# Kernel tuning notes

Hardware: AMD Instinct MI355X
Metric: run time of the kernel (lower is better)

The kernel has to match this reference:

```python
import jax, jax.numpy as jnp
import numpy as np

N_ATOMS = 768
BOX_L = 30.0
CUTOFF = 5.0


def _cp(a, b, c):
    # numpy equivalent of torch.cartesian_prod for 1-D inputs
    g = np.meshgrid(a, b, c, indexing='ij')
    return np.stack(g, axis=-1).reshape(-1, 3)


def get_shifts_np(box, pbc, cutoff):
    # host-side mirror of TorchNeighborList._get_shifts (data-dependent shapes)
    recip = np.linalg.inv(box).T
    inv_len = np.linalg.norm(recip, axis=1)
    nrep = np.where(pbc, np.ceil(cutoff * inv_len).astype(np.int64), 0)
    r1 = np.arange(1, nrep[0] + 1)
    r2 = np.arange(1, nrep[1] + 1)
    r3 = np.arange(1, nrep[2] + 1)
    o = np.zeros(1, dtype=np.int64)
    blocks = [_cp(r1, r2, r3), _cp(r1, r2, o), _cp(r1, r2, -r3),
              _cp(r1, o, r3), _cp(r1, o, o), _cp(r1, o, -r3),
              _cp(r1, -r2, r3), _cp(r1, -r2, o), _cp(r1, -r2, -r3),
              _cp(o, r2, r3), _cp(o, r2, o), _cp(o, r2, -r3), _cp(o, o, r3)]
    return np.concatenate(blocks, axis=0).astype(np.int32)


def setup_inputs() -> dict:
    key = jax.random.key(0)
    positions = jax.random.uniform(key, (N_ATOMS, 3), dtype=jnp.float32) * BOX_L
    box = jnp.eye(3, dtype=jnp.float32) * BOX_L
    shifts = jnp.asarray(get_shifts_np(np.eye(3) * BOX_L, np.array([True, True, True]), CUTOFF))  # (13, 3)
    return {"positions": positions, "box": box, "shifts": shifts, "cutoff": CUTOFF}


def reference(positions, box, shifts, cutoff):
    N = positions.shape[0]
    S = shifts.shape[0]
    # central-cell unique pairs i<j (torch.combinations)
    iu, ju = jnp.triu_indices(N, k=1)
    # shifted candidates: cartesian_prod(shift_index, i, j)
    shift_idx = jnp.repeat(jnp.arange(S), N * N)
    pi_s = jnp.tile(jnp.repeat(jnp.arange(N), N), S)
    pj_s = jnp.tile(jnp.arange(N), S * N)
    pi_all = jnp.concatenate([iu, pi_s])          # (P,)
    pj_all = jnp.concatenate([ju, pj_s])          # (P,)
    shifts_all = jnp.concatenate([jnp.zeros((iu.shape[0], 3), dtype=shifts.dtype), shifts[shift_idx]])  # (P,3)
    shift_vals = shifts_all.astype(box.dtype) @ box
    Rij = positions[pi_all] - positions[pj_all] + shift_vals  # (P,3)
    d = jnp.linalg.norm(Rij, axis=1)
    mask = d < cutoff
    # bidirectional pairs (torch.cat of (i,j) and (j,i)), offsets negated for the first half
    bi_i = jnp.concatenate([pi_all, pj_all])
    bi_j = jnp.concatenate([pj_all, pi_all])
    bi_off = jnp.concatenate([-shifts_all, shifts_all])
    bi_mask = jnp.concatenate([mask, mask])
    # jit-compatible compaction: sort by idx_i with invalid entries pushed to the end
    sort_key = jnp.where(bi_mask, bi_i, N)
    order = jnp.argsort(sort_key)  # jax sort is stable
    valid = bi_mask[order]
    idx_i = jnp.where(valid, bi_i[order], -1)
    idx_j = jnp.where(valid, bi_j[order], -1)
    offset = (bi_off[order].astype(box.dtype) @ box) * valid[:, None].astype(box.dtype)
    return idx_i, idx_j, offset, valid
```

## Files before the change

kernel.cpp:

```cpp
#include <hip/hip_runtime.h>

#pragma clang fp contract(off)


#define MAX_SHIFTS 64
#define NFB 4096

typedef float f32x4 __attribute__((ext_vector_type(4)));
typedef int i32x4 __attribute__((ext_vector_type(4)));

__device__ __forceinline__ bool pv_fwd(float fx, float fy, float fz,
                                       const float* __restrict__ pos, int j,
                                       float sx, float sy, float sz, float cutoff) {
  float dx = fx - pos[j * 3 + 0] + sx;
  float dy = fy - pos[j * 3 + 1] + sy;
  float dz = fz - pos[j * 3 + 2] + sz;
  float d2 = dx * dx + dy * dy + dz * dz;
  return sqrtf(d2) < cutoff;
}

__device__ __forceinline__ bool pv_bwd(const float* __restrict__ pos, int a,
                                       float fx, float fy, float fz,
                                       float sx, float sy, float sz, float cutoff) {
  float dx = pos[a * 3 + 0] - fx + sx;
  float dy = pos[a * 3 + 1] - fy + sy;
  float dz = pos[a * 3 + 2] - fz + sz;
  float d2 = dx * dx + dy * dy + dz * dz;
  return sqrtf(d2) < cutoff;
}

__device__ __forceinline__ bool axis_ok(float lo, float hi, float cutpad) {
  return (hi > -cutpad) && (lo < cutpad);
}

__global__ __launch_bounds__(256) void k_count(
    const float* __restrict__ pos, const float* __restrict__ box,
    const int* __restrict__ shifts, const float* __restrict__ cutp,
    int N, int S, int* __restrict__ count) {
  __shared__ float sv[MAX_SHIFTS * 3];
  __shared__ float bred[4][6];
  __shared__ int rf[4], rb[4];
  int atom = blockIdx.x;
  int t = threadIdx.x;
  int w = t >> 6;
  float cut = cutp[0];
  float cutpad = cut + fmaxf(cut * 1e-5f, 1e-5f);

  for (int s = t; s < S; s += 256) {
    float s0 = (float)shifts[s * 3 + 0];
    float s1 = (float)shifts[s * 3 + 1];
    float s2 = (float)shifts[s * 3 + 2];
    sv[s * 3 + 0] = s0 * box[0] + s1 * box[3] + s2 * box[6];
    sv[s * 3 + 1] = s0 * box[1] + s1 * box[4] + s2 * box[7];
    sv[s * 3 + 2] = s0 * box[2] + s1 * box[5] + s2 * box[8];
  }

  float mnx = 1e30f, mny = 1e30f, mnz = 1e30f, mxx = -1e30f, mxy = -1e30f, mxz = -1e30f;
  for (int i = t; i < N; i += 256) {
    float x = pos[3 * i + 0], y = pos[3 * i + 1], z = pos[3 * i + 2];
    mnx = fminf(mnx, x); mny = fminf(mny, y); mnz = fminf(mnz, z);
    mxx = fmaxf(mxx, x); mxy = fmaxf(mxy, y); mxz = fmaxf(mxz, z);
  }
  for (int off = 32; off; off >>= 1) {
    mnx = fminf(mnx, __shfl_xor(mnx, off)); mny = fminf(mny, __shfl_xor(mny, off));
    mnz = fminf(mnz, __shfl_xor(mnz, off)); mxx = fmaxf(mxx, __shfl_xor(mxx, off));
    mxy = fmaxf(mxy, __shfl_xor(mxy, off)); mxz = fmaxf(mxz, __shfl_xor(mxz, off));
  }
  if ((t & 63) == 0) {
    bred[w][0] = mnx; bred[w][1] = mny; bred[w][2] = mnz;
    bred[w][3] = mxx; bred[w][4] = mxy; bred[w][5] = mxz;
  }
  __syncthreads();
  mnx = bred[0][0]; mny = bred[0][1]; mnz = bred[0][2];
  mxx = bred[0][3]; mxy = bred[0][4]; mxz = bred[0][5];
  for (int ww = 1; ww < 4; ww++) {
    mnx = fminf(mnx, bred[ww][0]); mny = fminf(mny, bred[ww][1]); mnz = fminf(mnz, bred[ww][2]);
    mxx = fmaxf(mxx, bred[ww][3]); mxy = fmaxf(mxy, bred[ww][4]); mxz = fmaxf(mxz, bred[ww][5]);
  }

  float pix = pos[3 * atom + 0], piy = pos[3 * atom + 1], piz = pos[3 * atom + 2];
  int cf = 0, cb = 0;
  for (int j = atom + 1 + t; j < N; j += 256)
    if (pv_fwd(pix, piy, piz, pos, j, 0.f, 0.f, 0.f, cut)) cf++;
  for (int a = t; a < atom; a += 256)
    if (pv_bwd(pos, a, pix, piy, piz, 0.f, 0.f, 0.f, cut)) cb++;

  for (int s = 0; s < S; s++) {
    float svx = sv[3 * s + 0], svy = sv[3 * s + 1], svz = sv[3 * s + 2];
    bool af = axis_ok((pix - mxx) + svx, (pix - mnx) + svx, cutpad) &&
              axis_ok((piy - mxy) + svy, (piy - mny) + svy, cutpad) &&
              axis_ok((piz - mxz) + svz, (piz - mnz) + svz, cutpad);
    if (af) {
      for (int j = t; j < N; j += 256)
        if (pv_fwd(pix, piy, piz, pos, j, svx, svy, svz, cut)) cf++;
    }
    bool ab = axis_ok((mnx - pix) + svx, (mxx - pix) + svx, cutpad) &&
              axis_ok((mny - piy) + svy, (mxy - piy) + svy, cutpad) &&
              axis_ok((mnz - piz) + svz, (mxz - piz) + svz, cutpad);
    if (ab) {
      for (int a = t; a < N; a += 256)
        if (pv_bwd(pos, a, pix, piy, piz, svx, svy, svz, cut)) cb++;
    }
  }
  for (int off = 32; off; off >>= 1) {
    cf += __shfl_down(cf, off);
    cb += __shfl_down(cb, off);
  }
  if ((t & 63) == 0) { rf[w] = cf; rb[w] = cb; }
  __syncthreads();
  if (t == 0) {
    count[2 * atom + 0] = rf[0] + rf[1] + rf[2] + rf[3];
    count[2 * atom + 1] = rb[0] + rb[1] + rb[2] + rb[3];
  }
}

__global__ __launch_bounds__(256) void k_main(
    const float* __restrict__ pos, const float* __restrict__ box,
    const int* __restrict__ shifts, const float* __restrict__ cutp,
    int N, int S, const int* __restrict__ count,
    float* __restrict__ out, long M, long n4, int NWB) {
  __shared__ float sv[MAX_SHIFTS * 3];
  int t = threadIdx.x;
  int lane = t & 63, w = t >> 6;
  int n2 = 2 * N;

  if ((int)blockIdx.x < NWB) {
    float cut = cutp[0];
    float cutpad = cut + fmaxf(cut * 1e-5f, 1e-5f);
    for (int s = t; s < S; s += 256) {
      float s0 = (float)shifts[s * 3 + 0];
      float s1 = (float)shifts[s * 3 + 1];
      float s2 = (float)shifts[s * 3 + 2];
      sv[s * 3 + 0] = s0 * box[0] + s1 * box[3] + s2 * box[6];
      sv[s * 3 + 1] = s0 * box[1] + s1 * box[4] + s2 * box[7];
      sv[s * 3 + 2] = s0 * box[2] + s1 * box[5] + s2 * box[8];
    }
    __syncthreads();
    int g = blockIdx.x * 4 + w;
    if (g >= n2) return;
    int atom = g >> 1;
    int dir = g & 1;

    float mnx = 1e30f, mny = 1e30f, mnz = 1e30f, mxx = -1e30f, mxy = -1e30f, mxz = -1e30f;
    for (int i = lane; i < N; i += 64) {
      float x = pos[3 * i + 0], y = pos[3 * i + 1], z = pos[3 * i + 2];
      mnx = fminf(mnx, x); mny = fminf(mny, y); mnz = fminf(mnz, z);
      mxx = fmaxf(mxx, x); mxy = fmaxf(mxy, y); mxz = fmaxf(mxz, z);
    }
    for (int off = 32; off; off >>= 1) {
      mnx = fminf(mnx, __shfl_xor(mnx, off)); mny = fminf(mny, __shfl_xor(mny, off));
      mnz = fminf(mnz, __shfl_xor(mnz, off)); mxx = fmaxf(mxx, __shfl_xor(mxx, off));
      mxy = fmaxf(mxy, __shfl_xor(mxy, off)); mxz = fmaxf(mxz, __shfl_xor(mxz, off));
    }

    int pre = 0;
    for (int i = lane; i < g; i += 64) pre += count[i];
    for (int off = 32; off; off >>= 1) pre += __shfl_xor(pre, off);
    long base = pre;

    float* __restrict__ out_i = out;
    float* __restrict__ out_j = out + M;
    float* __restrict__ out_off = out + 2 * M;
    float* __restrict__ out_v = out + 5 * M;

    float pix = pos[3 * atom + 0], piy = pos[3 * atom + 1], piz = pos[3 * atom + 2];
    float fatom = (float)atom;
    float cut2 = cut;
    int running = 0;

    {
      int n = (dir == 0) ? (N - 1 - atom) : atom;
      int j0 = (dir == 0) ? (atom + 1) : 0;
      float oz0 = (dir == 0) ? -0.0f : 0.0f;
      for (int c0 = 0; c0 < n; c0 += 64) {
        int c = c0 + lane;
        bool v = false;
        int other = j0 + c;
        if (c < n) {
          v = (dir == 0) ? pv_fwd(pix, piy, piz, pos, other, 0.f, 0.f, 0.f, cut2)
                         : pv_bwd(pos, other, pix, piy, piz, 0.f, 0.f, 0.f, cut2);
        }
        unsigned long long m = __ballot(v);
        if (v) {
          int rank = __popcll(m & ((1ULL << lane) - 1ULL));
          long row = base + running + rank;
          out_i[row] = fatom;
          out_j[row] = (float)other;
          out_off[row * 3 + 0] = oz0;
          out_off[row * 3 + 1] = oz0;
          out_off[row * 3 + 2] = oz0;
          out_v[row] = 1.0f;
        }
        running += __popcll(m);
      }
    }
    for (int s = 0; s < S; s++) {
      float svx = sv[3 * s + 0], svy = sv[3 * s + 1], svz = sv[3 * s + 2];
      bool active;
      if (dir == 0) {
        active = axis_ok((pix - mxx) + svx, (pix - mnx) + svx, cutpad) &&
                 axis_ok((piy - mxy) + svy, (piy - mny) + svy, cutpad) &&
                 axis_ok((piz - mxz) + svz, (piz - mnz) + svz, cutpad);
      } else {
        active = axis_ok((mnx - pix) + svx, (mxx - pix) + svx, cutpad) &&
                 axis_ok((mny - piy) + svy, (mxy - piy) + svy, cutpad) &&
                 axis_ok((mnz - piz) + svz, (mxz - piz) + svz, cutpad);
      }
      if (!active) continue;
      float ox = (dir == 0) ? -svx : svx;
      float oy = (dir == 0) ? -svy : svy;
      float oz = (dir == 0) ? -svz : svz;
      for (int c0 = 0; c0 < N; c0 += 64) {
        int other = c0 + lane;
        bool v = false;
        if (other < N) {
          v = (dir == 0) ? pv_fwd(pix, piy, piz, pos, other, svx, svy, svz, cut2)
                         : pv_bwd(pos, other, pix, piy, piz, svx, svy, svz, cut2);
        }
        unsigned long long m = __ballot(v);
        if (v) {
          int rank = __popcll(m & ((1ULL << lane) - 1ULL));
          long row = base + running + rank;
          out_i[row] = fatom;
          out_j[row] = (float)other;
          out_off[row * 3 + 0] = ox;
          out_off[row * 3 + 1] = oy;
          out_off[row * 3 + 2] = oz;
          out_v[row] = 1.0f;
        }
        running += __popcll(m);
      }
    }
  } else {
    int tot = 0;
    const i32x4* __restrict__ c4 = (const i32x4*)count;
    int nq = n2 >> 2;
    for (int i = lane; i < nq; i += 64) {
      i32x4 v = c4[i];
      tot += v.x + v.y + v.z + v.w;
    }
    for (int off = 32; off; off >>= 1) tot += __shfl_xor(tot, off);
    long total = tot;

    long E0 = total;
    long E1 = M + total;
    long E2 = 2 * M + 3 * total;
    long E3 = 5 * M + total;
    long m2 = 2 * M, m5 = 5 * M;
    const f32x4 neg = {-1.f, -1.f, -1.f, -1.f};
    const f32x4 zer = {0.f, 0.f, 0.f, 0.f};
    f32x4* __restrict__ out4 = (f32x4*)out;

    long fidx = ((long)blockIdx.x - NWB) * 256 + t;
    long fstride = (long)NFB * 256;
    for (long k = fidx; k < n4; k += fstride) {
      long e = k << 2;
      long ve = (e < M) ? E0 : ((e < m2) ? E1 : ((e < m5) ? E2 : E3));
      if (e + 4 <= ve) continue;
      bool isneg = (e < m2);
      if (e >= ve) {
        out4[k] = isneg ? neg : zer;
      } else {
        float dv = isneg ? -1.f : 0.f;
        for (int q = 0; q < 4; q++)
          if (e + q >= ve) out[e + q] = dv;
      }
    }
  }
}

extern "C" void kernel_launch(void* const* d_in, const int* in_sizes, int n_in,
                              void* d_out, int out_size, void* d_ws, size_t ws_size,
                              hipStream_t stream) {
  const float* pos = (const float*)d_in[0];
  const float* box = (const float*)d_in[1];
  const int* shifts = (const int*)d_in[2];
  const float* cutp = (const float*)d_in[3];
  int N = in_sizes[0] / 3;
  int S = in_sizes[2] / 3;
  long M = (long)out_size / 6;
  float* out = (float*)d_out;

  int* count = (int*)d_ws;

  long n4 = (long)out_size / 4;
  int NWB = (2 * N + 3) / 4;

  hipLaunchKernelGGL(k_count, dim3(N), dim3(256), 0, stream,
                     pos, box, shifts, cutp, N, S, count);
  hipLaunchKernelGGL(k_main, dim3(NWB + NFB), dim3(256), 0, stream,
                     pos, box, shifts, cutp, N, S, count, out, M, n4, NWB);
}
```

Baseline: 110.3 us.

## Reorder fill blocks first and give each a contiguous chunk with fast path

The fill blocks now come first in the grid, and there are fewer of them. Each one handles a contiguous, 256-aligned chunk of the output instead of grid-striding across the whole buffer. Chunks that do not overlap any valid region or segment boundary take a branch-free unrolled vector-store loop that writes a constant value. This cuts per-element branching and index arithmetic in the large padding fill and lets the fill start earlier. The risk is load imbalance across fewer blocks, and pair blocks that are scheduled later could lengthen the tail.

```diff
diff --git a/kernel.cpp b/kernel.cpp
--- a/kernel.cpp
+++ b/kernel.cpp
@@ -4,7 +4,7 @@
 
 
 #define MAX_SHIFTS 64
-#define NFB 4096
+#define NFB 512
 
 typedef float f32x4 __attribute__((ext_vector_type(4)));
 typedef int i32x4 __attribute__((ext_vector_type(4)));
@@ -118,120 +118,18 @@
     const float* __restrict__ pos, const float* __restrict__ box,
     const int* __restrict__ shifts, const float* __restrict__ cutp,
     int N, int S, const int* __restrict__ count,
-    float* __restrict__ out, long M, long n4, int NWB) {
+    float* __restrict__ out, long M, long n4, long chunk4) {
   __shared__ float sv[MAX_SHIFTS * 3];
   int t = threadIdx.x;
   int lane = t & 63, w = t >> 6;
   int n2 = 2 * N;
 
-  if ((int)blockIdx.x < NWB) {
-    float cut = cutp[0];
-    float cutpad = cut + fmaxf(cut * 1e-5f, 1e-5f);
-    for (int s = t; s < S; s += 256) {
-      float s0 = (float)shifts[s * 3 + 0];
-      float s1 = (float)shifts[s * 3 + 1];
-      float s2 = (float)shifts[s * 3 + 2];
-      sv[s * 3 + 0] = s0 * box[0] + s1 * box[3] + s2 * box[6];
-      sv[s * 3 + 1] = s0 * box[1] + s1 * box[4] + s2 * box[7];
-      sv[s * 3 + 2] = s0 * box[2] + s1 * box[5] + s2 * box[8];
-    }
-    __syncthreads();
-    int g = blockIdx.x * 4 + w;
-    if (g >= n2) return;
-    int atom = g >> 1;
-    int dir = g & 1;
-
-    float mnx = 1e30f, mny = 1e30f, mnz = 1e30f, mxx = -1e30f, mxy = -1e30f, mxz = -1e30f;
-    for (int i = lane; i < N; i += 64) {
-      float x = pos[3 * i + 0], y = pos[3 * i + 1], z = pos[3 * i + 2];
-      mnx = fminf(mnx, x); mny = fminf(mny, y); mnz = fminf(mnz, z);
-      mxx = fmaxf(mxx, x); mxy = fmaxf(mxy, y); mxz = fmaxf(mxz, z);
-    }
-    for (int off = 32; off; off >>= 1) {
-      mnx = fminf(mnx, __shfl_xor(mnx, off)); mny = fminf(mny, __shfl_xor(mny, off));
-      mnz = fminf(mnz, __shfl_xor(mnz, off)); mxx = fmaxf(mxx, __shfl_xor(mxx, off));
-      mxy = fmaxf(mxy, __shfl_xor(mxy, off)); mxz = fmaxf(mxz, __shfl_xor(mxz, off));
-    }
-
-    int pre = 0;
-    for (int i = lane; i < g; i += 64) pre += count[i];
-    for (int off = 32; off; off >>= 1) pre += __shfl_xor(pre, off);
-    long base = pre;
-
-    float* __restrict__ out_i = out;
-    float* __restrict__ out_j = out + M;
-    float* __restrict__ out_off = out + 2 * M;
-    float* __restrict__ out_v = out + 5 * M;
-
-    float pix = pos[3 * atom + 0], piy = pos[3 * atom + 1], piz = pos[3 * atom + 2];
-    float fatom = (float)atom;
-    float cut2 = cut;
-    int running = 0;
-
-    {
-      int n = (dir == 0) ? (N - 1 - atom) : atom;
-      int j0 = (dir == 0) ? (atom + 1) : 0;
-      float oz0 = (dir == 0) ? -0.0f : 0.0f;
-      for (int c0 = 0; c0 < n; c0 += 64) {
-        int c = c0 + lane;
-        bool v = false;
-        int other = j0 + c;
-        if (c < n) {
-          v = (dir == 0) ? pv_fwd(pix, piy, piz, pos, other, 0.f, 0.f, 0.f, cut2)
-                         : pv_bwd(pos, other, pix, piy, piz, 0.f, 0.f, 0.f, cut2);
-        }
-        unsigned long long m = __ballot(v);
-        if (v) {
-          int rank = __popcll(m & ((1ULL << lane) - 1ULL));
-          long row = base + running + rank;
-          out_i[row] = fatom;
-          out_j[row] = (float)other;
-          out_off[row * 3 + 0] = oz0;
-          out_off[row * 3 + 1] = oz0;
-          out_off[row * 3 + 2] = oz0;
-          out_v[row] = 1.0f;
-        }
-        running += __popcll(m);
-      }
-    }
-    for (int s = 0; s < S; s++) {
-      float svx = sv[3 * s + 0], svy = sv[3 * s + 1], svz = sv[3 * s + 2];
-      bool active;
-      if (dir == 0) {
-        active = axis_ok((pix - mxx) + svx, (pix - mnx) + svx, cutpad) &&
-                 axis_ok((piy - mxy) + svy, (piy - mny) + svy, cutpad) &&
-                 axis_ok((piz - mxz) + svz, (piz - mnz) + svz, cutpad);
-      } else {
-        active = axis_ok((mnx - pix) + svx, (mxx - pix) + svx, cutpad) &&
-                 axis_ok((mny - piy) + svy, (mxy - piy) + svy, cutpad) &&
-                 axis_ok((mnz - piz) + svz, (mxz - piz) + svz, cutpad);
-      }
-      if (!active) continue;
-      float ox = (dir == 0) ? -svx : svx;
-      float oy = (dir == 0) ? -svy : svy;
-      float oz = (dir == 0) ? -svz : svz;
-      for (int c0 = 0; c0 < N; c0 += 64) {
-        int other = c0 + lane;
-        bool v = false;
-        if (other < N) {
-          v = (dir == 0) ? pv_fwd(pix, piy, piz, pos, other, svx, svy, svz, cut2)
-                         : pv_bwd(pos, other, pix, piy, piz, svx, svy, svz, cut2);
-        }
-        unsigned long long m = __ballot(v);
-        if (v) {
-          int rank = __popcll(m & ((1ULL << lane) - 1ULL));
-          long row = base + running + rank;
-          out_i[row] = fatom;
-          out_j[row] = (float)other;
-          out_off[row * 3 + 0] = ox;
-          out_off[row * 3 + 1] = oy;
-          out_off[row * 3 + 2] = oz;
-          out_v[row] = 1.0f;
-        }
-        running += __popcll(m);
-      }
-    }
-  } else {
+  if ((int)blockIdx.x < NFB) {
+    long k_lo = (long)blockIdx.x * chunk4;
+    long k_hi = k_lo + chunk4;
+    if (k_hi > n4) k_hi = n4;
+    if (k_lo >= k_hi) return;
+
     int tot = 0;
     const i32x4* __restrict__ c4 = (const i32x4*)count;
     int nq = n2 >> 2;
@@ -251,20 +149,141 @@
     const f32x4 zer = {0.f, 0.f, 0.f, 0.f};
     f32x4* __restrict__ out4 = (f32x4*)out;
 
-    long fidx = ((long)blockIdx.x - NWB) * 256 + t;
-    long fstride = (long)NFB * 256;
-    for (long k = fidx; k < n4; k += fstride) {
-      long e = k << 2;
-      long ve = (e < M) ? E0 : ((e < m2) ? E1 : ((e < m5) ? E2 : E3));
-      if (e + 4 <= ve) continue;
-      bool isneg = (e < m2);
-      if (e >= ve) {
-        out4[k] = isneg ? neg : zer;
-      } else {
-        float dv = isneg ? -1.f : 0.f;
-        for (int q = 0; q < 4; q++)
-          if (e + q >= ve) out[e + q] = dv;
-      }
+    long e_lo = k_lo << 2, e_hi = k_hi << 2;
+    bool crosses = (e_lo < m2) && (e_hi > m2);
+    bool ov = (e_lo < E0) ||
+              (e_hi > M && e_lo < E1) ||
+              (e_hi > m2 && e_lo < E2) ||
+              (e_hi > m5 && e_lo < E3);
+
+    if (!crosses && !ov) {
+      f32x4 val = (e_lo < m2) ? neg : zer;
+      f32x4* __restrict__ p = out4 + k_lo + t;
+      long iters = (k_hi - k_lo) >> 8;
+#pragma unroll 8
+      for (long it = 0; it < iters; it++) p[it * 256] = val;
+      for (long k = k_lo + (iters << 8) + t; k < k_hi; k += 256) out4[k] = (k << 2) < m2 ? neg : zer;
+    } else {
+      for (long k = k_lo + t; k < k_hi; k += 256) {
+        long e = k << 2;
+        long ve = (e < M) ? E0 : ((e < m2) ? E1 : ((e < m5) ? E2 : E3));
+        if (e + 4 <= ve) continue;
+        bool isneg = (e < m2);
+        if (e >= ve) {
+          out4[k] = isneg ? neg : zer;
+        } else {
+          float dv = isneg ? -1.f : 0.f;
+          for (int q = 0; q < 4; q++)
+            if (e + q >= ve) out[e + q] = dv;
+        }
+      }
+    }
+    return;
+  }
+
+  float cut = cutp[0];
+  float cutpad = cut + fmaxf(cut * 1e-5f, 1e-5f);
+  for (int s = t; s < S; s += 256) {
+    float s0 = (float)shifts[s * 3 + 0];
+    float s1 = (float)shifts[s * 3 + 1];
+    float s2 = (float)shifts[s * 3 + 2];
+    sv[s * 3 + 0] = s0 * box[0] + s1 * box[3] + s2 * box[6];
+    sv[s * 3 + 1] = s0 * box[1] + s1 * box[4] + s2 * box[7];
+    sv[s * 3 + 2] = s0 * box[2] + s1 * box[5] + s2 * box[8];
+  }
+  __syncthreads();
+  int g = ((int)blockIdx.x - NFB) * 4 + w;
+  if (g >= n2) return;
+  int atom = g >> 1;
+  int dir = g & 1;
+
+  float mnx = 1e30f, mny = 1e30f, mnz = 1e30f, mxx = -1e30f, mxy = -1e30f, mxz = -1e30f;
+  for (int i = lane; i < N; i += 64) {
+    float x = pos[3 * i + 0], y = pos[3 * i + 1], z = pos[3 * i + 2];
+    mnx = fminf(mnx, x); mny = fminf(mny, y); mnz = fminf(mnz, z);
+    mxx = fmaxf(mxx, x); mxy = fmaxf(mxy, y); mxz = fmaxf(mxz, z);
+  }
+  for (int off = 32; off; off >>= 1) {
+    mnx = fminf(mnx, __shfl_xor(mnx, off)); mny = fminf(mny, __shfl_xor(mny, off));
+    mnz = fminf(mnz, __shfl_xor(mnz, off)); mxx = fmaxf(mxx, __shfl_xor(mxx, off));
+    mxy = fmaxf(mxy, __shfl_xor(mxy, off)); mxz = fmaxf(mxz, __shfl_xor(mxz, off));
+  }
+
+  int pre = 0;
+  for (int i = lane; i < g; i += 64) pre += count[i];
+  for (int off = 32; off; off >>= 1) pre += __shfl_xor(pre, off);
+  long base = pre;
+
+  float* __restrict__ out_i = out;
+  float* __restrict__ out_j = out + M;
+  float* __restrict__ out_off = out + 2 * M;
+  float* __restrict__ out_v = out + 5 * M;
+
+  float pix = pos[3 * atom + 0], piy = pos[3 * atom + 1], piz = pos[3 * atom + 2];
+  float fatom = (float)atom;
+  int running = 0;
+
+  {
+    int n = (dir == 0) ? (N - 1 - atom) : atom;
+    int j0 = (dir == 0) ? (atom + 1) : 0;
+    float oz0 = (dir == 0) ? -0.0f : 0.0f;
+    for (int c0 = 0; c0 < n; c0 += 64) {
+      int c = c0 + lane;
+      bool v = false;
+      int other = j0 + c;
+      if (c < n) {
+        v = (dir == 0) ? pv_fwd(pix, piy, piz, pos, other, 0.f, 0.f, 0.f, cut)
+                       : pv_bwd(pos, other, pix, piy, piz, 0.f, 0.f, 0.f, cut);
+      }
+      unsigned long long m = __ballot(v);
+      if (v) {
+        int rank = __popcll(m & ((1ULL << lane) - 1ULL));
+        long row = base + running + rank;
+        out_i[row] = fatom;
+        out_j[row] = (float)other;
+        out_off[row * 3 + 0] = oz0;
+        out_off[row * 3 + 1] = oz0;
+        out_off[row * 3 + 2] = oz0;
+        out_v[row] = 1.0f;
+      }
+      running += __popcll(m);
+    }
+  }
+  for (int s = 0; s < S; s++) {
+    float svx = sv[3 * s + 0], svy = sv[3 * s + 1], svz = sv[3 * s + 2];
+    bool active;
+    if (dir == 0) {
+      active = axis_ok((pix - mxx) + svx, (pix - mnx) + svx, cutpad) &&
+               axis_ok((piy - mxy) + svy, (piy - mny) + svy, cutpad) &&
+               axis_ok((piz - mxz) + svz, (piz - mnz) + svz, cutpad);
+    } else {
+      active = axis_ok((mnx - pix) + svx, (mxx - pix) + svx, cutpad) &&
+               axis_ok((mny - piy) + svy, (mxy - piy) + svy, cutpad) &&
+               axis_ok((mnz - piz) + svz, (mxz - piz) + svz, cutpad);
+    }
+    if (!active) continue;
+    float ox = (dir == 0) ? -svx : svx;
+    float oy = (dir == 0) ? -svy : svy;
+    float oz = (dir == 0) ? -svz : svz;
+    for (int c0 = 0; c0 < N; c0 += 64) {
+      int other = c0 + lane;
+      bool v = false;
+      if (other < N) {
+        v = (dir == 0) ? pv_fwd(pix, piy, piz, pos, other, svx, svy, svz, cut)
+                       : pv_bwd(pos, other, pix, piy, piz, svx, svy, svz, cut);
+      }
+      unsigned long long m = __ballot(v);
+      if (v) {
+        int rank = __popcll(m & ((1ULL << lane) - 1ULL));
+        long row = base + running + rank;
+        out_i[row] = fatom;
+        out_j[row] = (float)other;
+        out_off[row * 3 + 0] = ox;
+        out_off[row * 3 + 1] = oy;
+        out_off[row * 3 + 2] = oz;
+        out_v[row] = 1.0f;
+      }
+      running += __popcll(m);
     }
   }
 }
@@ -284,10 +303,11 @@
   int* count = (int*)d_ws;
 
   long n4 = (long)out_size / 4;
+  long chunk4 = ((n4 + NFB - 1) / NFB + 255) / 256 * 256;
   int NWB = (2 * N + 3) / 4;
 
   hipLaunchKernelGGL(k_count, dim3(N), dim3(256), 0, stream,
                      pos, box, shifts, cutp, N, S, count);
-  hipLaunchKernelGGL(k_main, dim3(NWB + NFB), dim3(256), 0, stream,
-                     pos, box, shifts, cutp, N, S, count, out, M, n4, NWB);
-}
+  hipLaunchKernelGGL(k_main, dim3(NFB + NWB), dim3(256), 0, stream,
+                     pos, box, shifts, cutp, N, S, count, out, M, n4, chunk4);
+}
```

Result: no change. 109.8 us (-0.4%).
